# Kernel tuning notes

Hardware: AMD Instinct MI355X
Metric: run time of the kernel (lower is better)

## Reference

```python
import jax, jax.numpy as jnp
import numpy as np

# static config (matches init_kwargs / input_specs)
T, B, CIN, H, W = 48, 64, 1, 64, 64
OC, KH, KW, STRIDE = 16, 7, 7, 2
N, P = 1000, 4
ALPHA, BETA, TH = 0.9, 0.9, 1.0
HO = (H - KH) // STRIDE + 1  # 29
WO = (W - KW) // STRIDE + 1  # 29
IN_SZ = OC * HO * WO         # 13456
SURR_ALPHA = 2.0             # snntorch default ATan surrogate alpha


@jax.custom_vjp
def atan_spike(x):
    # Heaviside forward, ATan surrogate backward (snntorch default spike_grad)
    return (x > 0).astype(x.dtype)

def _atan_fwd(x):
    return atan_spike(x), x

def _atan_bwd(x, g):
    return (g * (SURR_ALPHA / 2.0) / (1.0 + (jnp.pi / 2.0 * SURR_ALPHA * x) ** 2),)

atan_spike.defvjp(_atan_fwd, _atan_bwd)


def setup_inputs() -> dict:
    key = jax.random.key(0)
    ks = jax.random.split(key, 6)
    x = jax.random.normal(ks[0], (T, B, CIN, H, W), dtype=jnp.float32)
    gabor_w = jax.random.normal(ks[1], (OC, CIN, KH, KW), dtype=jnp.float32) * 0.3
    Wins = jax.random.normal(ks[2], (P, N, IN_SZ), dtype=jnp.float32) * (1.0 / np.sqrt(IN_SZ))
    fc1_b = jax.random.normal(ks[3], (N,), dtype=jnp.float32) * 0.01
    Wlsm = jax.random.normal(ks[4], (N, N), dtype=jnp.float32) * (0.5 / np.sqrt(N))
    rec_b = jax.random.normal(ks[5], (N,), dtype=jnp.float32) * 0.01
    return {"x": x, "gabor_w": gabor_w, "Wins": Wins, "fc1_b": fc1_b, "Wlsm": Wlsm, "rec_b": rec_b}


def _forward(x, gabor_w, Wins, fc1_b, Wlsm, rec_b):
    # Gabor conv on all timesteps at once (conv has no recurrent dependence)
    xt = x.reshape(T * B, CIN, H, W)
    g = jax.lax.conv_general_dilated(
        xt, gabor_w, window_strides=(STRIDE, STRIDE), padding="VALID",
        dimension_numbers=("NCHW", "OIHW", "NCHW"))          # [T*B, OC, HO, WO]
    feat = g.reshape(P, T // P, B, IN_SZ)
    curr = jnp.einsum("ptbi,pni->ptbn", feat, Wins).reshape(T, B, N) + fc1_b

    # RSynaptic recurrence (snntorch, reset_mechanism='subtract'):
    #   reset = H(mem_prev - th)            (detached)
    #   syn   = alpha*syn + curr + V @ spk_prev + b
    #   mem   = beta*mem + syn - reset*th
    #   spk   = H(mem - th)                 (ATan surrogate grad)
    def step(state, c):
        spk, syn, mem = state
        reset = jax.lax.stop_gradient((mem - TH > 0).astype(mem.dtype))
        syn = ALPHA * syn + c + spk @ Wlsm.T + rec_b
        mem = BETA * mem + syn - reset * TH
        spk = atan_spike(mem - TH)
        return (spk, syn, mem), spk

    z = jnp.zeros((B, N), dtype=curr.dtype)
    _, spk_rec = jax.lax.scan(step, (z, z, z), curr)
    return spk_rec  # [T, B, N]


def reference(x, gabor_w, Wins, fc1_b, Wlsm, rec_b):
    return _forward(x, gabor_w, Wins, fc1_b, Wlsm, rec_b)
```

## Files before the change

### kernel.cpp

```cpp
#include <hip/hip_runtime.h>
#include <hip/hip_bf16.h>

#define T_STEPS 48
#define B_SZ    64
#define H_IN    64
#define W_IN    64
#define OC      16
#define KH      7
#define KW      7
#define STRIDEC 2
#define HO      29
#define WO      29
#define IN_SZ   13456
#define N_NEU   1000
#define N_PAD   1024

#define WT_OFF    0ull
#define CURR_OFF  4096000ull
#define SYN_OFF   16678912ull
#define MEM_OFF   16941056ull
#define MASK_OFF  17203200ull
#define G_OFF     17219584ull

__global__ __launch_bounds__(256) void transpose_wlsm(const float* __restrict__ Wlsm,
                                                      float* __restrict__ WT) {
  __shared__ float t[32][33];
  const int m0 = blockIdx.x * 32;
  const int n0 = blockIdx.y * 32;
  const int tx = threadIdx.x & 31, ty = threadIdx.x >> 5;
  #pragma unroll
  for (int j = 0; j < 4; ++j) {
    int n = n0 + ty + j * 8, m = m0 + tx;
    t[ty + j * 8][tx] = (n < N_NEU && m < N_NEU) ? Wlsm[n * N_NEU + m] : 0.f;
  }
  __syncthreads();
  #pragma unroll
  for (int j = 0; j < 4; ++j) {
    int m = m0 + ty + j * 8, n = n0 + tx;
    if (m < N_NEU) WT[(size_t)m * N_PAD + n] = t[tx][ty + j * 8];
  }
}

__global__ __launch_bounds__(256) void conv_kernel(const float* __restrict__ x,
                                                   const float* __restrict__ w,
                                                   float* __restrict__ g,
                                                   int img0) {
  __shared__ float img[H_IN * W_IN];
  const int blk = blockIdx.x;
  const float* xim = x + (size_t)(img0 + blk) * (H_IN * W_IN);
  for (int i = threadIdx.x; i < (H_IN * W_IN) / 4; i += 256)
    ((float4*)img)[i] = ((const float4*)xim)[i];
  __syncthreads();
  float* gout = g + (size_t)blk * IN_SZ;
  for (int pos = threadIdx.x; pos < HO * WO; pos += 256) {
    const int oh = pos / WO, ow = pos - oh * WO;
    const int ih = oh * STRIDEC, iw = ow * STRIDEC;
    float acc[OC];
    #pragma unroll
    for (int oc = 0; oc < OC; ++oc) acc[oc] = 0.f;
    #pragma unroll
    for (int kh = 0; kh < KH; ++kh) {
      #pragma unroll
      for (int kw = 0; kw < KW; ++kw) {
        const float v = img[(ih + kh) * W_IN + iw + kw];
        const int widx = kh * KW + kw;
        #pragma unroll
        for (int oc = 0; oc < OC; ++oc)
          acc[oc] += v * w[oc * (KH * KW) + widx];
      }
    }
    #pragma unroll
    for (int oc = 0; oc < OC; ++oc)
      gout[oc * (HO * WO) + pos] = acc[oc];
  }
}

#define BM3 128
#define BN3 64
#define BK3 32
#define LDA3 132
#define LDB3 68
__global__ __launch_bounds__(256) void gemm_kernel(const float* __restrict__ A,
                                                   int row_off,
                                                   const float* __restrict__ Wins,
                                                   const float* __restrict__ fc1_b,
                                                   float* __restrict__ curr) {
  __shared__ __align__(16) float As[BK3 * LDA3];
  __shared__ __align__(16) float Bs[BK3 * LDB3];
  const int tid = threadIdx.x;
  const int n0 = blockIdx.x * BN3;
  const int row_l0 = blockIdx.y * BM3;
  const int r0 = (tid >> 4) * 8;
  const int c0 = (tid & 15) * 4;
  const int p = (row_off + row_l0) / 768;
  const float* Bp = Wins + (size_t)p * N_NEU * IN_SZ;

  float acc[8][4];
  #pragma unroll
  for (int i = 0; i < 8; ++i)
    #pragma unroll
    for (int j = 0; j < 4; ++j) acc[i][j] = 0.f;

  for (int k0 = 0; k0 < IN_SZ; k0 += BK3) {
    #pragma unroll
    for (int it = 0; it < 4; ++it) {
      const int f = it * 256 + tid;
      const int rr = f >> 3;
      const int kq = (f & 7) * 4;
      const int k = k0 + kq;
      float4 va = make_float4(0.f, 0.f, 0.f, 0.f);
      if (k < IN_SZ)
        va = *(const float4*)(A + (size_t)(row_l0 + rr) * IN_SZ + k);
      As[(kq + 0) * LDA3 + rr] = va.x;
      As[(kq + 1) * LDA3 + rr] = va.y;
      As[(kq + 2) * LDA3 + rr] = va.z;
      As[(kq + 3) * LDA3 + rr] = va.w;
    }
    #pragma unroll
    for (int it = 0; it < 2; ++it) {
      const int f = it * 256 + tid;
      const int cc = f >> 3;
      const int kq = (f & 7) * 4;
      const int k = k0 + kq;
      float4 vb = make_float4(0.f, 0.f, 0.f, 0.f);
      if (k < IN_SZ && n0 + cc < N_NEU)
        vb = *(const float4*)(Bp + (size_t)(n0 + cc) * IN_SZ + k);
      Bs[(kq + 0) * LDB3 + cc] = vb.x;
      Bs[(kq + 1) * LDB3 + cc] = vb.y;
      Bs[(kq + 2) * LDB3 + cc] = vb.z;
      Bs[(kq + 3) * LDB3 + cc] = vb.w;
    }
    __syncthreads();

    float lacc[8][4];
    #pragma unroll
    for (int i = 0; i < 8; ++i)
      #pragma unroll
      for (int j = 0; j < 4; ++j) lacc[i][j] = 0.f;
    #pragma unroll
    for (int kk = 0; kk < BK3; ++kk) {
      const float4 a0 = *(const float4*)&As[kk * LDA3 + r0];
      const float4 a1 = *(const float4*)&As[kk * LDA3 + r0 + 4];
      const float4 b0 = *(const float4*)&Bs[kk * LDB3 + c0];
      const float a[8] = {a0.x, a0.y, a0.z, a0.w, a1.x, a1.y, a1.z, a1.w};
      const float bb[4] = {b0.x, b0.y, b0.z, b0.w};
      #pragma unroll
      for (int i = 0; i < 8; ++i)
        #pragma unroll
        for (int j = 0; j < 4; ++j) lacc[i][j] += a[i] * bb[j];
    }
    #pragma unroll
    for (int i = 0; i < 8; ++i)
      #pragma unroll
      for (int j = 0; j < 4; ++j) acc[i][j] += lacc[i][j];
    __syncthreads();
  }

  const int g_row_base = row_off + row_l0 + r0;
  #pragma unroll
  for (int i = 0; i < 8; ++i) {
    float* crow = curr + ((size_t)(g_row_base + i) << 10);
    float4 o;
    const int nn = n0 + c0;
    o.x = acc[i][0] + fc1_b[nn + 0 < N_NEU ? nn + 0 : (N_NEU - 1)];
    o.y = acc[i][1] + fc1_b[nn + 1 < N_NEU ? nn + 1 : (N_NEU - 1)];
    o.z = acc[i][2] + fc1_b[nn + 2 < N_NEU ? nn + 2 : (N_NEU - 1)];
    o.w = acc[i][3] + fc1_b[nn + 3 < N_NEU ? nn + 3 : (N_NEU - 1)];
    *(float4*)(crow + nn) = o;
  }
}

__global__ __launch_bounds__(256) void step_kernel(
    const float* __restrict__ WT, const float* __restrict__ curr_t,
    const float* __restrict__ rec_b, float* __restrict__ syn,
    float* __restrict__ mem_s, const unsigned long long* __restrict__ mask_rd,
    unsigned long long* __restrict__ mask_wr, float* __restrict__ out_t) {
  __shared__ int idxs[1024];
  __shared__ int cnts[16];
  __shared__ int offs[17];
  __shared__ float4 red[256];
  __shared__ unsigned char nib[32];
  const int tid = threadIdx.x;
  const int b = blockIdx.x >> 3;
  const int e = blockIdx.x & 7;

  if (tid < 16) cnts[tid] = (int)__popcll(mask_rd[(b << 4) | tid]);
  __syncthreads();
  if (tid == 0) {
    int o = 0;
    #pragma unroll
    for (int c = 0; c < 16; ++c) { offs[c] = o; o += cnts[c]; }
    offs[16] = o;
  }
  __syncthreads();
  if (tid < 16) {
    unsigned long long s = mask_rd[(b << 4) | tid];
    int o = offs[tid];
    const int base = tid << 6;
    while (s) {
      idxs[o++] = base + __builtin_ctzll(s);
      s &= s - 1;
    }
  }
  __syncthreads();
  const int L = offs[16];

  const int g = tid >> 5;
  const int ln = tid & 31;
  const float* wc = WT + e * 128 + ln * 4;
  float4 acc = make_float4(0.f, 0.f, 0.f, 0.f);
  int j = g;
  for (; j + 16 <= L; j += 16) {
    const float4 v0 = *(const float4*)(wc + ((size_t)idxs[j] << 10));
    const float4 v1 = *(const float4*)(wc + ((size_t)idxs[j + 8] << 10));
    acc.x += v0.x; acc.y += v0.y; acc.z += v0.z; acc.w += v0.w;
    acc.x += v1.x; acc.y += v1.y; acc.z += v1.z; acc.w += v1.w;
  }
  for (; j < L; j += 8) {
    const float4 v = *(const float4*)(wc + ((size_t)idxs[j] << 10));
    acc.x += v.x; acc.y += v.y; acc.z += v.z; acc.w += v.w;
  }
  red[tid] = acc;
  __syncthreads();

  if (tid < 32) {
    float4 rec = red[tid];
    #pragma unroll
    for (int h = 1; h < 8; ++h) {
      const float4 v = red[h * 32 + tid];
      rec.x += v.x; rec.y += v.y; rec.z += v.z; rec.w += v.w;
    }
    const int n = e * 128 + tid * 4;
    const size_t idx = ((size_t)b << 10) + n;
    const float4 cv = *(const float4*)(curr_t + idx);
    float4 sv = *(float4*)(syn + idx);
    float4 mv = *(float4*)(mem_s + idx);
    const float rb0 = (n + 0 < N_NEU) ? rec_b[n + 0] : 0.f;
    const float rb1 = (n + 1 < N_NEU) ? rec_b[n + 1] : 0.f;
    const float rb2 = (n + 2 < N_NEU) ? rec_b[n + 2] : 0.f;
    const float rb3 = (n + 3 < N_NEU) ? rec_b[n + 3] : 0.f;
    float4 sn, mn;
    sn.x = 0.9f * sv.x + cv.x + rec.x + rb0;
    sn.y = 0.9f * sv.y + cv.y + rec.y + rb1;
    sn.z = 0.9f * sv.z + cv.z + rec.z + rb2;
    sn.w = 0.9f * sv.w + cv.w + rec.w + rb3;
    mn.x = 0.9f * mv.x + sn.x - ((mv.x - 1.0f > 0.f) ? 1.0f : 0.f);
    mn.y = 0.9f * mv.y + sn.y - ((mv.y - 1.0f > 0.f) ? 1.0f : 0.f);
    mn.z = 0.9f * mv.z + sn.z - ((mv.z - 1.0f > 0.f) ? 1.0f : 0.f);
    mn.w = 0.9f * mv.w + sn.w - ((mv.w - 1.0f > 0.f) ? 1.0f : 0.f);
    *(float4*)(syn + idx) = sn;
    *(float4*)(mem_s + idx) = mn;
    const int s0 = ((mn.x - 1.0f) > 0.f && n + 0 < N_NEU) ? 1 : 0;
    const int s1 = ((mn.y - 1.0f) > 0.f && n + 1 < N_NEU) ? 1 : 0;
    const int s2 = ((mn.z - 1.0f) > 0.f && n + 2 < N_NEU) ? 1 : 0;
    const int s3 = ((mn.w - 1.0f) > 0.f && n + 3 < N_NEU) ? 1 : 0;
    if (n + 0 < N_NEU) out_t[b * N_NEU + n + 0] = (float)s0;
    if (n + 1 < N_NEU) out_t[b * N_NEU + n + 1] = (float)s1;
    if (n + 2 < N_NEU) out_t[b * N_NEU + n + 2] = (float)s2;
    if (n + 3 < N_NEU) out_t[b * N_NEU + n + 3] = (float)s3;
    nib[tid] = (unsigned char)(s0 | (s1 << 1) | (s2 << 2) | (s3 << 3));
  }
  __syncthreads();
  if (tid < 2) {
    unsigned long long w = 0;
    #pragma unroll
    for (int i = 0; i < 16; ++i)
      w |= (unsigned long long)nib[tid * 16 + i] << (4 * i);
    mask_wr[(b << 4) | (e * 2 + tid)] = w;
  }
}

extern "C" void kernel_launch(void* const* d_in, const int* in_sizes, int n_in,
                              void* d_out, int out_size, void* d_ws, size_t ws_size,
                              hipStream_t stream) {
  const float* x     = (const float*)d_in[0];
  const float* gw    = (const float*)d_in[1];
  const float* Wins  = (const float*)d_in[2];
  const float* fc1_b = (const float*)d_in[3];
  const float* Wlsm  = (const float*)d_in[4];
  const float* rec_b = (const float*)d_in[5];
  float* out = (float*)d_out;
  char* ws = (char*)d_ws;

  float* WT   = (float*)(ws + WT_OFF);
  float* curr = (float*)(ws + CURR_OFF);
  float* syn  = (float*)(ws + SYN_OFF);
  float* mem  = (float*)(ws + MEM_OFF);
  unsigned long long* mask = (unsigned long long*)(ws + MASK_OFF);
  float* gbuf = (float*)(ws + G_OFF);

  (void)hipMemsetAsync(ws + SYN_OFF, 0, (size_t)(MASK_OFF - SYN_OFF) + 16384, stream);

  hipLaunchKernelGGL(transpose_wlsm, dim3(32, 32), dim3(256), 0, stream, Wlsm, WT);

  const size_t needA = G_OFF + (size_t)3072 * IN_SZ * 4;
  if (ws_size >= needA) {
    hipLaunchKernelGGL(conv_kernel, dim3(3072), dim3(256), 0, stream, x, gw, gbuf, 0);
    hipLaunchKernelGGL(gemm_kernel, dim3(16, 24), dim3(256), 0, stream,
                       gbuf, 0, Wins, fc1_b, curr);
  } else {
    for (int p = 0; p < 4; ++p) {
      hipLaunchKernelGGL(conv_kernel, dim3(768), dim3(256), 0, stream,
                         x, gw, gbuf, p * 768);
      hipLaunchKernelGGL(gemm_kernel, dim3(16, 6), dim3(256), 0, stream,
                         gbuf, p * 768, Wins, fc1_b, curr);
    }
  }

  for (int t = 0; t < T_STEPS; ++t) {
    hipLaunchKernelGGL(step_kernel, dim3(512), dim3(256), 0, stream,
                       WT, curr + (size_t)t * 65536, rec_b, syn, mem,
                       mask + (size_t)(t & 1) * 1024,
                       mask + (size_t)((t + 1) & 1) * 1024,
                       out + (size_t)t * 64000);
  }
}
```

Baseline: 2.950 ms.

## Double-buffer GEMM shared tiles with register prefetch; unroll spike gather loop

```diff
diff --git a/kernel.cpp b/kernel.cpp
--- a/kernel.cpp
+++ b/kernel.cpp
@@ -80,13 +80,68 @@
 #define BK3 32
 #define LDA3 132
 #define LDB3 68
+#define NT3 421
+
+__device__ __forceinline__ void gemm_load(const float* __restrict__ A,
+                                          const float* __restrict__ Bp,
+                                          int row_l0, int n0, int k0, int tid,
+                                          float4* rva, float4* rvb) {
+  #pragma unroll
+  for (int it = 0; it < 4; ++it) {
+    const int f = it * 256 + tid;
+    const int rr = f >> 3;
+    const int kq = (f & 7) * 4;
+    const int k = k0 + kq;
+    float4 v = make_float4(0.f, 0.f, 0.f, 0.f);
+    if (k < IN_SZ)
+      v = *(const float4*)(A + (size_t)(row_l0 + rr) * IN_SZ + k);
+    rva[it] = v;
+  }
+  #pragma unroll
+  for (int it = 0; it < 2; ++it) {
+    const int f = it * 256 + tid;
+    const int cc = f >> 3;
+    const int kq = (f & 7) * 4;
+    const int k = k0 + kq;
+    float4 v = make_float4(0.f, 0.f, 0.f, 0.f);
+    if (k < IN_SZ && n0 + cc < N_NEU)
+      v = *(const float4*)(Bp + (size_t)(n0 + cc) * IN_SZ + k);
+    rvb[it] = v;
+  }
+}
+
+__device__ __forceinline__ void gemm_write(float* __restrict__ as,
+                                           float* __restrict__ bs, int tid,
+                                           const float4* rva, const float4* rvb) {
+  #pragma unroll
+  for (int it = 0; it < 4; ++it) {
+    const int f = it * 256 + tid;
+    const int rr = f >> 3;
+    const int kq = (f & 7) * 4;
+    as[(kq + 0) * LDA3 + rr] = rva[it].x;
+    as[(kq + 1) * LDA3 + rr] = rva[it].y;
+    as[(kq + 2) * LDA3 + rr] = rva[it].z;
+    as[(kq + 3) * LDA3 + rr] = rva[it].w;
+  }
+  #pragma unroll
+  for (int it = 0; it < 2; ++it) {
+    const int f = it * 256 + tid;
+    const int cc = f >> 3;
+    const int kq = (f & 7) * 4;
+    bs[(kq + 0) * LDB3 + cc] = rvb[it].x;
+    bs[(kq + 1) * LDB3 + cc] = rvb[it].y;
+    bs[(kq + 2) * LDB3 + cc] = rvb[it].z;
+    bs[(kq + 3) * LDB3 + cc] = rvb[it].w;
+  }
+}
+
 __global__ __launch_bounds__(256) void gemm_kernel(const float* __restrict__ A,
                                                    int row_off,
                                                    const float* __restrict__ Wins,
                                                    const float* __restrict__ fc1_b,
                                                    float* __restrict__ curr) {
-  __shared__ __align__(16) float As[BK3 * LDA3];
-  __shared__ __align__(16) float Bs[BK3 * LDB3];
+  __shared__ __align__(16) float As[2][BK3 * LDA3];
+  __shared__ __align__(16) float Bs[2][BK3 * LDB3];
   const int tid = threadIdx.x;
   const int n0 = blockIdx.x * BN3;
   const int row_l0 = blockIdx.y * BM3;
@@ -95,43 +150,24 @@
   const int p = (row_off + row_l0) / 768;
   const float* Bp = Wins + (size_t)p * N_NEU * IN_SZ;
 
+  float4 rva[4], rvb[2];
   float acc[8][4];
   #pragma unroll
   for (int i = 0; i < 8; ++i)
     #pragma unroll
     for (int j = 0; j < 4; ++j) acc[i][j] = 0.f;
 
-  for (int k0 = 0; k0 < IN_SZ; k0 += BK3) {
-    #pragma unroll
-    for (int it = 0; it < 4; ++it) {
-      const int f = it * 256 + tid;
-      const int rr = f >> 3;
-      const int kq = (f & 7) * 4;
-      const int k = k0 + kq;
-      float4 va = make_float4(0.f, 0.f, 0.f, 0.f);
-      if (k < IN_SZ)
-        va = *(const float4*)(A + (size_t)(row_l0 + rr) * IN_SZ + k);
-      As[(kq + 0) * LDA3 + rr] = va.x;
-      As[(kq + 1) * LDA3 + rr] = va.y;
-      As[(kq + 2) * LDA3 + rr] = va.z;
-      As[(kq + 3) * LDA3 + rr] = va.w;
-    }
-    #pragma unroll
-    for (int it = 0; it < 2; ++it) {
-      const int f = it * 256 + tid;
-      const int cc = f >> 3;
-      const int kq = (f & 7) * 4;
-      const int k = k0 + kq;
-      float4 vb = make_float4(0.f, 0.f, 0.f, 0.f);
-      if (k < IN_SZ && n0 + cc < N_NEU)
-        vb = *(const float4*)(Bp + (size_t)(n0 + cc) * IN_SZ + k);
-      Bs[(kq + 0) * LDB3 + cc] = vb.x;
-      Bs[(kq + 1) * LDB3 + cc] = vb.y;
-      Bs[(kq + 2) * LDB3 + cc] = vb.z;
-      Bs[(kq + 3) * LDB3 + cc] = vb.w;
-    }
-    __syncthreads();
-
+  gemm_load(A, Bp, row_l0, n0, 0, tid, rva, rvb);
+  gemm_write(As[0], Bs[0], tid, rva, rvb);
+  __syncthreads();
+  int cur = 0;
+
+  for (int t = 0; t < NT3; ++t) {
+    if (t + 1 < NT3)
+      gemm_load(A, Bp, row_l0, n0, (t + 1) * BK3, tid, rva, rvb);
+
+    const float* as = As[cur];
+    const float* bs = Bs[cur];
     float lacc[8][4];
     #pragma unroll
     for (int i = 0; i < 8; ++i)
@@ -139,9 +175,9 @@
       for (int j = 0; j < 4; ++j) lacc[i][j] = 0.f;
     #pragma unroll
     for (int kk = 0; kk < BK3; ++kk) {
-      const float4 a0 = *(const float4*)&As[kk * LDA3 + r0];
-      const float4 a1 = *(const float4*)&As[kk * LDA3 + r0 + 4];
-      const float4 b0 = *(const float4*)&Bs[kk * LDB3 + c0];
+      const float4 a0 = *(const float4*)&as[kk * LDA3 + r0];
+      const float4 a1 = *(const float4*)&as[kk * LDA3 + r0 + 4];
+      const float4 b0 = *(const float4*)&bs[kk * LDB3 + c0];
       const float a[8] = {a0.x, a0.y, a0.z, a0.w, a1.x, a1.y, a1.z, a1.w};
       const float bb[4] = {b0.x, b0.y, b0.z, b0.w};
       #pragma unroll
@@ -153,7 +189,12 @@
     for (int i = 0; i < 8; ++i)
       #pragma unroll
       for (int j = 0; j < 4; ++j) acc[i][j] += lacc[i][j];
-    __syncthreads();
+
+    if (t + 1 < NT3) {
+      gemm_write(As[cur ^ 1], Bs[cur ^ 1], tid, rva, rvb);
+      __syncthreads();
+      cur ^= 1;
+    }
   }
 
   const int g_row_base = row_off + row_l0 + r0;
@@ -210,6 +251,16 @@
   const float* wc = WT + e * 128 + ln * 4;
   float4 acc = make_float4(0.f, 0.f, 0.f, 0.f);
   int j = g;
+  for (; j + 32 <= L; j += 32) {
+    const float4 v0 = *(const float4*)(wc + ((size_t)idxs[j] << 10));
+    const float4 v1 = *(const float4*)(wc + ((size_t)idxs[j + 8] << 10));
+    const float4 v2 = *(const float4*)(wc + ((size_t)idxs[j + 16] << 10));
+    const float4 v3 = *(const float4*)(wc + ((size_t)idxs[j + 24] << 10));
+    acc.x += v0.x; acc.y += v0.y; acc.z += v0.z; acc.w += v0.w;
+    acc.x += v1.x; acc.y += v1.y; acc.z += v1.z; acc.w += v1.w;
+    acc.x += v2.x; acc.y += v2.y; acc.z += v2.z; acc.w += v2.w;
+    acc.x += v3.x; acc.y += v3.y; acc.z += v3.z; acc.w += v3.w;
+  }
   for (; j + 16 <= L; j += 16) {
     const float4 v0 = *(const float4*)(wc + ((size_t)idxs[j] << 10));
     const float4 v1 = *(const float4*)(wc + ((size_t)idxs[j + 8] << 10));
```

Result: slower. 3.597 ms (+22.0%).
